# Kernel tuning notes

Measured on AMD Instinct MI355X. Metric: run time of the kernel, lower is better.

Reference implementation:

```python
import jax, jax.numpy as jnp
import numpy as np

D = 256          # input_dim (node embedding dim)
ATT_TIMES = 2
ATT_NUM = 2
DIN = D * ATT_NUM  # NTN input dim = 512
F = 16           # feature_map_dim


def setup_inputs() -> dict:
    key = jax.random.key(0)
    ks = jax.random.split(key, 10)
    x1 = jax.random.normal(ks[0], (120000, D), dtype=jnp.float32)
    x2 = jax.random.normal(ks[1], (100000, D), dtype=jnp.float32)
    # attention weight (glorot)
    W0 = jax.random.normal(ks[2], (D, D), dtype=jnp.float32) * (2.0 / (D + D)) ** 0.5
    # NTN params
    V = jax.random.normal(ks[3], (F, 2 * DIN), dtype=jnp.float32) * (2.0 / (F + 2 * DIN)) ** 0.5
    W = jax.random.normal(ks[4], (F, DIN, DIN), dtype=jnp.float32) * (2.0 / (DIN + DIN)) ** 0.5
    b = jax.random.normal(ks[5], (F,), dtype=jnp.float32)
    # projection MLP 16->8->4->2->1, torch Linear weights are (out, in)
    P0 = jax.random.normal(ks[6], (8, 16), dtype=jnp.float32) * (2.0 / (8 + 16)) ** 0.5
    P1 = jax.random.normal(ks[7], (4, 8), dtype=jnp.float32) * (2.0 / (4 + 8)) ** 0.5
    P2 = jax.random.normal(ks[8], (2, 4), dtype=jnp.float32) * (2.0 / (2 + 4)) ** 0.5
    P3 = jax.random.normal(ks[9], (1, 2), dtype=jnp.float32) * (2.0 / (1 + 2)) ** 0.5
    return {"x1": x1, "x2": x2, "W0": W0, "V": V, "W": W, "b": b,
            "P0": P0, "P1": P1, "P2": P2, "P3": P3}


def _attention(x, W0):
    # x: (N, D) -> (1, D*ATT_NUM) graph embedding.
    outs = []
    for _ in range(ATT_NUM):  # 'dot' style: same params each head (eye W), kept for faithfulness
        cur = x
        out = None
        for _ in range(ATT_TIMES):
            temp = jnp.mean(cur, axis=0, keepdims=True)          # (1, D)
            h_avg = jnp.tanh(temp @ W0)                          # att_weight=True
            att = jax.nn.sigmoid(cur @ h_avg.T)                  # (N, 1), W=eye in 'dot' style
            out = att.T @ cur                                    # (1, D)
            cur = cur * att
        outs.append(out)
    return jnp.concatenate(outs, axis=1)                         # (1, DIN)


def _ntn(g1, g2, V, W, b):
    # g1, g2: (1, DIN). Fused bilinear over all F feature maps.
    concat = jnp.concatenate([g1, g2], axis=1)                   # (1, 2*DIN)
    v_term = concat @ V.T                                        # (1, F)
    w_term = jnp.einsum('nd,fde,me->nf', g1, W, g2)              # (1, F)
    return jax.nn.sigmoid(v_term + w_term + b)                   # inneract = sigmoid


def reference(x1, x2, W0, V, W, b, P0, P1, P2, P3):
    g1 = _attention(x1, W0)
    g2 = _attention(x2, W0)
    x = _ntn(g1, g2, V, W, b)                                    # (1, F), branch 'an'
    for P in (P0, P1, P2, P3):                                   # Linear(no bias) + Sigmoid
        x = jax.nn.sigmoid(x @ P.T)
    return x                                                     # (1, 1)
```

## Files before the change

kernel.cpp:

```cpp
#include <hip/hip_runtime.h>
#include <math.h>

#define DD 256
#define REPS 8

#define OFF_SUMREP 0
#define OFF_H1P    4096
#define OFF_S1REP  4608
#define OFF_H2P    8704
#define OFF_OREP   9216
#define OFF_WTREP  13824
#define WS_FLOATS  13952
#define MIRROR_OFF_BYTES 65536

typedef float    f32x4 __attribute__((ext_vector_type(4)));
typedef float    f32x8 __attribute__((ext_vector_type(8)));
typedef _Float16 f16x4 __attribute__((ext_vector_type(4)));
typedef _Float16 f16x8 __attribute__((ext_vector_type(8)));

__device__ __forceinline__ float sigmoidf_(float x) { return 1.0f / (1.0f + __expf(-x)); }

__device__ __forceinline__ f32x8 ld8(const f16x8* p, size_t i) {
    return __builtin_convertvector(p[i], f32x8);
}
__device__ __forceinline__ f32x8 ld8(const f32x8* p, size_t i) { return p[i]; }

__device__ __forceinline__ float dot8(f32x8 a, f32x8 b) {
    f32x8 m = a * b;
    return ((m[0] + m[4]) + (m[1] + m[5])) + ((m[2] + m[6]) + (m[3] + m[7]));
}

__global__ void k_zero(float* __restrict__ ws) {
    int i = blockIdx.x * 256 + threadIdx.x;
    if (i < WS_FLOATS) ws[i] = 0.0f;
}

__device__ __forceinline__ void block_reduce_atomic4(f32x4 acc, int t, float* dst_base) {
    __shared__ f32x4 lds[256];
    lds[t] = acc;
    __syncthreads();
    if (t < 64) {
        f32x4 s = lds[t] + lds[t + 64] + lds[t + 128] + lds[t + 192];
        float* dst = dst_base + t * 4;
        atomicAdd(dst + 0, s.x); atomicAdd(dst + 1, s.y);
        atomicAdd(dst + 2, s.z); atomicAdd(dst + 3, s.w);
    }
}

__device__ __forceinline__ void block_reduce_atomic8(f32x8 acc, int t, float* dst_base) {
    __shared__ f32x8 lds8[256];
    lds8[t] = acc;
    __syncthreads();
    const float* lf = (const float*)lds8;
    float s = 0.f;
#pragma unroll
    for (int slot = 0; slot < 8; slot++) s += lf[slot * 256 + t];
    atomicAdd(dst_base + t, s);
}

template<bool WM>
__global__ void k_mean_t(const f32x4* __restrict__ x1, const f32x4* __restrict__ x2,
                         f16x4* __restrict__ m1, f16x4* __restrict__ m2,
                         int N1, int N2, float* __restrict__ ws) {
    int b = blockIdx.x, t = threadIdx.x;
    int inp = (b < 1024) ? 0 : 1;
    int bl = inp ? (b - 1024) : b;
    const f32x4* x = inp ? x2 : x1;
    f16x4* mm = inp ? m2 : m1;
    int N = inp ? N2 : N1;
    int col4 = t & 63, rg = t >> 6;
    int wid = bl * 4 + rg;
    const int S = 4096;
    f32x4 acc = {0.f, 0.f, 0.f, 0.f};
    int r = wid;
    for (; r + 3 * S < N; r += 4 * S) {
        size_t i0 = (size_t)r * 64 + col4;
        f32x4 v0 = x[i0];
        f32x4 v1 = x[i0 + (size_t)S * 64];
        f32x4 v2 = x[i0 + (size_t)2 * S * 64];
        f32x4 v3 = x[i0 + (size_t)3 * S * 64];
        if (WM) {
            mm[i0]                   = __builtin_convertvector(v0, f16x4);
            mm[i0 + (size_t)S * 64]  = __builtin_convertvector(v1, f16x4);
            mm[i0 + (size_t)2*S*64]  = __builtin_convertvector(v2, f16x4);
            mm[i0 + (size_t)3*S*64]  = __builtin_convertvector(v3, f16x4);
        }
        acc += (v0 + v1) + (v2 + v3);
    }
    for (; r < N; r += S) {
        size_t i0 = (size_t)r * 64 + col4;
        f32x4 v = x[i0];
        if (WM) mm[i0] = __builtin_convertvector(v, f16x4);
        acc += v;
    }
    block_reduce_atomic4(acc, t, ws + OFF_SUMREP + inp * (REPS * 256) + (bl & (REPS - 1)) * 256);
}

__global__ void k_hpart(const float* __restrict__ W0, float* __restrict__ ws,
                        int srcOff, int dstOff, int N1, int N2) {
    int inp = blockIdx.x >> 4, g = blockIdx.x & 15;
    int t = threadIdx.x;
    __shared__ float temp[16];
    if (t < 16) {
        const float* src = ws + srcOff + inp * (REPS * 256) + g * 16 + t;
        float s = 0.f;
#pragma unroll
        for (int r = 0; r < REPS; r++) s += src[r * 256];
        temp[t] = s * (1.0f / (float)(inp ? N2 : N1));
    }
    __syncthreads();
    float p = 0.f;
#pragma unroll
    for (int j = 0; j < 16; j++) p += temp[j] * W0[(g * 16 + j) * 256 + t];
    atomicAdd(ws + dstOff + inp * 256 + t, p);
}

template<typename T>
__global__ void k_att1_t(const T* __restrict__ b1, const T* __restrict__ b2,
                         int N1, int N2, float* __restrict__ ws) {
    int b = blockIdx.x, t = threadIdx.x;
    int inp = (b < 1024) ? 0 : 1;
    int bl = inp ? (b - 1024) : b;
    const T* x = inp ? b2 : b1;
    int N = inp ? N2 : N1;
    int lane = t & 63, w = t >> 6;
    int half = lane >> 5, l32 = lane & 31;
    f32x8 h1;
#pragma unroll
    for (int j = 0; j < 8; j++) h1[j] = tanhf(ws[OFF_H1P + inp * 256 + l32 * 8 + j]);
    f32x8 acc = {0.f, 0.f, 0.f, 0.f, 0.f, 0.f, 0.f, 0.f};
    int wid = bl * 4 + w;
    const int PS = 8192;
    int base = wid * 2;
    for (; base + PS + 1 < N; base += 2 * PS) {
        f32x8 va = ld8(x, (size_t)(base + half) * 32 + l32);
        f32x8 vb = ld8(x, (size_t)(base + PS + half) * 32 + l32);
        float da = dot8(va, h1), db = dot8(vb, h1);
#pragma unroll
        for (int off = 16; off; off >>= 1) {
            da += __shfl_xor(da, off, 64);
            db += __shfl_xor(db, off, 64);
        }
        acc += sigmoidf_(da) * va + sigmoidf_(db) * vb;
    }
    for (; base + 1 < N; base += PS) {
        f32x8 v = ld8(x, (size_t)(base + half) * 32 + l32);
        float d = dot8(v, h1);
#pragma unroll
        for (int off = 16; off; off >>= 1) d += __shfl_xor(d, off, 64);
        acc += sigmoidf_(d) * v;
    }
    if (base < N && half == 0) {
        f32x8 v = ld8(x, (size_t)base * 32 + l32);
        float d = dot8(v, h1);
#pragma unroll
        for (int off = 16; off; off >>= 1) d += __shfl_xor(d, off, 64);
        acc += sigmoidf_(d) * v;
    }
    block_reduce_atomic8(acc, t, ws + OFF_S1REP + inp * (REPS * 256) + (bl & (REPS - 1)) * 256);
}

template<typename T>
__global__ void k_att2_t(const T* __restrict__ b1, const T* __restrict__ b2,
                         int N1, int N2, float* __restrict__ ws) {
    int b = blockIdx.x, t = threadIdx.x;
    int inp = (b < 1024) ? 0 : 1;
    int bl = inp ? (b - 1024) : b;
    const T* x = inp ? b2 : b1;
    int N = inp ? N2 : N1;
    int lane = t & 63, w = t >> 6;
    int half = lane >> 5, l32 = lane & 31;
    f32x8 h1, h2;
#pragma unroll
    for (int j = 0; j < 8; j++) {
        h1[j] = tanhf(ws[OFF_H1P + inp * 256 + l32 * 8 + j]);
        h2[j] = tanhf(ws[OFF_H2P + inp * 256 + l32 * 8 + j]);
    }
    f32x8 acc = {0.f, 0.f, 0.f, 0.f, 0.f, 0.f, 0.f, 0.f};
    int wid = bl * 4 + w;
    const int PS = 8192;
    int base = wid * 2;
    for (; base + PS + 1 < N; base += 2 * PS) {
        f32x8 va = ld8(x, (size_t)(base + half) * 32 + l32);
        f32x8 vb = ld8(x, (size_t)(base + PS + half) * 32 + l32);
        float da = dot8(va, h1), ea = dot8(va, h2);
        float db = dot8(vb, h1), eb = dot8(vb, h2);
#pragma unroll
        for (int off = 16; off; off >>= 1) {
            da += __shfl_xor(da, off, 64); ea += __shfl_xor(ea, off, 64);
            db += __shfl_xor(db, off, 64); eb += __shfl_xor(eb, off, 64);
        }
        float a1a = sigmoidf_(da);
        float a1b = sigmoidf_(db);
        acc += (a1a * sigmoidf_(a1a * ea)) * va + (a1b * sigmoidf_(a1b * eb)) * vb;
    }
    for (; base + 1 < N; base += PS) {
        f32x8 v = ld8(x, (size_t)(base + half) * 32 + l32);
        float d = dot8(v, h1), e = dot8(v, h2);
#pragma unroll
        for (int off = 16; off; off >>= 1) {
            d += __shfl_xor(d, off, 64); e += __shfl_xor(e, off, 64);
        }
        float a1 = sigmoidf_(d);
        acc += (a1 * sigmoidf_(a1 * e)) * v;
    }
    if (base < N && half == 0) {
        f32x8 v = ld8(x, (size_t)base * 32 + l32);
        float d = dot8(v, h1), e = dot8(v, h2);
#pragma unroll
        for (int off = 16; off; off >>= 1) {
            d += __shfl_xor(d, off, 64); e += __shfl_xor(e, off, 64);
        }
        float a1 = sigmoidf_(d);
        acc += (a1 * sigmoidf_(a1 * e)) * v;
    }
    block_reduce_atomic8(acc, t, ws + OFF_OREP + inp * (REPS * 256) + (bl & (REPS - 1)) * 256);
}

__global__ void __launch_bounds__(256, 4)
k_ntn(const float* __restrict__ W, float* __restrict__ ws) {
    __shared__ __align__(16) float o_l[512];
    int b = blockIdx.x, t = threadIdx.x;
    {
        float s0 = 0.f, s1 = 0.f;
#pragma unroll
        for (int r2 = 0; r2 < REPS; r2++) {
            s0 += ws[OFF_OREP + r2 * 256 + t];
            s1 += ws[OFF_OREP + REPS * 256 + r2 * 256 + t];
        }
        o_l[t] = s0; o_l[256 + t] = s1;
    }
    __syncthreads();
    int lane = t & 63, w = t >> 6;
    f32x4 o2f = ((const f32x4*)(o_l + 256))[lane];
    int g = b * 4 + w;
    const f32x4* W4 = (const f32x4*)W;
    float wt[4];
    int fidx[4];
#pragma unroll
    for (int u = 0; u < 4; u++) {
        int row = g + u * 2048;
        const f32x4* q = W4 + (size_t)row * 128 + lane;
        f32x4 m = (q[0] + q[64]) * o2f;
        float p = (m.x + m.y) + (m.z + m.w);
#pragma unroll
        for (int off = 32; off; off >>= 1) p += __shfl_xor(p, off, 64);
        wt[u] = o_l[row & 255] * p;
        fidx[u] = row >> 9;
    }
    if (lane == 0) {
        float* dst = ws + OFF_WTREP + (b & (REPS - 1)) * 16;
#pragma unroll
        for (int u = 0; u < 4; u++) atomicAdd(dst + fidx[u], wt[u]);
    }
}

__global__ void k_final(const float* __restrict__ V, const float* __restrict__ bb,
                        const float* __restrict__ P0, const float* __restrict__ P1,
                        const float* __restrict__ P2, const float* __restrict__ P3,
                        float* __restrict__ ws, float* __restrict__ out) {
    int t = threadIdx.x;
    __shared__ float o_l[512];
    {
        float s0 = 0.f, s1 = 0.f;
#pragma unroll
        for (int r2 = 0; r2 < REPS; r2++) {
            s0 += ws[OFF_OREP + r2 * 256 + t];
            s1 += ws[OFF_OREP + REPS * 256 + r2 * 256 + t];
        }
        o_l[t] = s0; o_l[256 + t] = s1;
    }
    __syncthreads();
    int f = t >> 4, j = t & 15;
    float p = 0.f;
    for (int k = j; k < 1024; k += 16) {
        float cv = (k < 512) ? o_l[k & 255] : o_l[256 + (k & 255)];
        p += cv * V[f * 1024 + k];
    }
    __shared__ float red[256];
    __shared__ float sv[16];
    red[t] = p;
    __syncthreads();
    if (t < 16) {
        float v = 0.f;
#pragma unroll
        for (int q = 0; q < 16; q++) v += red[t * 16 + q];
        float wt = 0.f;
#pragma unroll
        for (int r = 0; r < REPS; r++) wt += ws[OFF_WTREP + r * 16 + t];
        sv[t] = sigmoidf_(v + wt + bb[t]);
    }
    __syncthreads();
    if (t == 0) {
        float y0[8], y1[4], y2[2];
#pragma unroll
        for (int i = 0; i < 8; i++) {
            float s = 0.f;
            for (int k = 0; k < 16; k++) s += P0[i * 16 + k] * sv[k];
            y0[i] = sigmoidf_(s);
        }
#pragma unroll
        for (int i = 0; i < 4; i++) {
            float s = 0.f;
            for (int k = 0; k < 8; k++) s += P1[i * 8 + k] * y0[k];
            y1[i] = sigmoidf_(s);
        }
#pragma unroll
        for (int i = 0; i < 2; i++) {
            float s = 0.f;
            for (int k = 0; k < 4; k++) s += P2[i * 4 + k] * y1[k];
            y2[i] = sigmoidf_(s);
        }
        out[0] = sigmoidf_(P3[0] * y2[0] + P3[1] * y2[1]);
    }
}

extern "C" void kernel_launch(void* const* d_in, const int* in_sizes, int n_in,
                              void* d_out, int out_size, void* d_ws, size_t ws_size,
                              hipStream_t stream) {
    const float* x1 = (const float*)d_in[0];
    const float* x2 = (const float*)d_in[1];
    const float* W0 = (const float*)d_in[2];
    const float* V  = (const float*)d_in[3];
    const float* W  = (const float*)d_in[4];
    const float* b  = (const float*)d_in[5];
    const float* P0 = (const float*)d_in[6];
    const float* P1 = (const float*)d_in[7];
    const float* P2 = (const float*)d_in[8];
    const float* P3 = (const float*)d_in[9];
    float* ws  = (float*)d_ws;
    float* out = (float*)d_out;
    int N1 = in_sizes[0] / DD;
    int N2 = in_sizes[1] / DD;

    const f32x4* x1v = (const f32x4*)x1;
    const f32x4* x2v = (const f32x4*)x2;
    f16x4* m1 = (f16x4*)((char*)d_ws + MIRROR_OFF_BYTES);
    f16x4* m2 = m1 + (size_t)N1 * 64;
    size_t need = (size_t)MIRROR_OFF_BYTES + ((size_t)N1 + N2) * DD * sizeof(_Float16);
    bool use_mirror = ws_size >= need;

    k_zero <<<55, 256, 0, stream>>>(ws);
    if (use_mirror) {
        k_mean_t<true>  <<<2048, 256, 0, stream>>>(x1v, x2v, m1, m2, N1, N2, ws);
        k_hpart         <<<32,   256, 0, stream>>>(W0, ws, OFF_SUMREP, OFF_H1P, N1, N2);
        k_att1_t<f16x8> <<<2048, 256, 0, stream>>>((const f16x8*)m1, (const f16x8*)m2, N1, N2, ws);
        k_hpart         <<<32,   256, 0, stream>>>(W0, ws, OFF_S1REP, OFF_H2P, N1, N2);
        k_att2_t<f16x8> <<<2048, 256, 0, stream>>>((const f16x8*)m1, (const f16x8*)m2, N1, N2, ws);
    } else {
        k_mean_t<false> <<<2048, 256, 0, stream>>>(x1v, x2v, nullptr, nullptr, N1, N2, ws);
        k_hpart         <<<32,   256, 0, stream>>>(W0, ws, OFF_SUMREP, OFF_H1P, N1, N2);
        k_att1_t<f32x8> <<<2048, 256, 0, stream>>>((const f32x8*)x1, (const f32x8*)x2, N1, N2, ws);
        k_hpart         <<<32,   256, 0, stream>>>(W0, ws, OFF_S1REP, OFF_H2P, N1, N2);
        k_att2_t<f32x8> <<<2048, 256, 0, stream>>>((const f32x8*)x1, (const f32x8*)x2, N1, N2, ws);
    }
    k_ntn  <<<512, 256, 0, stream>>>(W, ws);
    k_final<<<1,   256, 0, stream>>>(V, b, P0, P1, P2, P3, ws, out);
}
```

Measured before the change: 415.0 us.

## Give each block a contiguous row chunk in mean and attention passes

Replaces grid-strided row assignment, where consecutive blocks interleave rows across the whole matrix, with a contiguous chunk of about N/1024 rows per block in the mean, att1 and att2 kernels. Each block streams one contiguous region, which is meant to improve DRAM page and cache locality. The att1 loop is also unrolled to four rows per wave per iteration to put more loads in flight. The cost is a little extra bounds arithmetic per block and possible imbalance when N is not a multiple of 1024.

Result: no change. 418.9 us (+1.0%).

```diff
diff --git a/kernel.cpp b/kernel.cpp
--- a/kernel.cpp
+++ b/kernel.cpp
@@ -68,26 +68,28 @@
     const f32x4* x = inp ? x2 : x1;
     f16x4* mm = inp ? m2 : m1;
     int N = inp ? N2 : N1;
+    int C = (N + 1023) >> 10;
+    int r0 = bl * C;
+    int r1 = r0 + C; if (r1 > N) r1 = N;
+    if (r0 > N) r0 = N;
     int col4 = t & 63, rg = t >> 6;
-    int wid = bl * 4 + rg;
-    const int S = 4096;
     f32x4 acc = {0.f, 0.f, 0.f, 0.f};
-    int r = wid;
-    for (; r + 3 * S < N; r += 4 * S) {
+    int r = r0 + rg;
+    for (; r + 12 < r1; r += 16) {
         size_t i0 = (size_t)r * 64 + col4;
         f32x4 v0 = x[i0];
-        f32x4 v1 = x[i0 + (size_t)S * 64];
-        f32x4 v2 = x[i0 + (size_t)2 * S * 64];
-        f32x4 v3 = x[i0 + (size_t)3 * S * 64];
+        f32x4 v1 = x[i0 + 256];
+        f32x4 v2 = x[i0 + 512];
+        f32x4 v3 = x[i0 + 768];
         if (WM) {
-            mm[i0]                   = __builtin_convertvector(v0, f16x4);
-            mm[i0 + (size_t)S * 64]  = __builtin_convertvector(v1, f16x4);
-            mm[i0 + (size_t)2*S*64]  = __builtin_convertvector(v2, f16x4);
-            mm[i0 + (size_t)3*S*64]  = __builtin_convertvector(v3, f16x4);
+            mm[i0]       = __builtin_convertvector(v0, f16x4);
+            mm[i0 + 256] = __builtin_convertvector(v1, f16x4);
+            mm[i0 + 512] = __builtin_convertvector(v2, f16x4);
+            mm[i0 + 768] = __builtin_convertvector(v3, f16x4);
         }
         acc += (v0 + v1) + (v2 + v3);
     }
-    for (; r < N; r += S) {
+    for (; r < r1; r += 4) {
         size_t i0 = (size_t)r * 64 + col4;
         f32x4 v = x[i0];
         if (WM) mm[i0] = __builtin_convertvector(v, f16x4);
@@ -123,35 +125,37 @@
     int bl = inp ? (b - 1024) : b;
     const T* x = inp ? b2 : b1;
     int N = inp ? N2 : N1;
+    int C = (N + 1023) >> 10;
+    int r0 = bl * C;
+    int r1 = r0 + C; if (r1 > N) r1 = N;
+    if (r0 > N) r0 = N;
     int lane = t & 63, w = t >> 6;
     int half = lane >> 5, l32 = lane & 31;
     f32x8 h1;
 #pragma unroll
     for (int j = 0; j < 8; j++) h1[j] = tanhf(ws[OFF_H1P + inp * 256 + l32 * 8 + j]);
     f32x8 acc = {0.f, 0.f, 0.f, 0.f, 0.f, 0.f, 0.f, 0.f};
-    int wid = bl * 4 + w;
-    const int PS = 8192;
-    int base = wid * 2;
-    for (; base + PS + 1 < N; base += 2 * PS) {
-        f32x8 va = ld8(x, (size_t)(base + half) * 32 + l32);
-        f32x8 vb = ld8(x, (size_t)(base + PS + half) * 32 + l32);
+    int rr = r0;
+    for (; rr + 32 <= r1; rr += 32) {
+        int ra = rr + 2 * w + half;
+        f32x8 va = ld8(x, (size_t)ra * 32 + l32);
+        f32x8 vb = ld8(x, (size_t)(ra + 8) * 32 + l32);
+        f32x8 vc = ld8(x, (size_t)(ra + 16) * 32 + l32);
+        f32x8 vd = ld8(x, (size_t)(ra + 24) * 32 + l32);
         float da = dot8(va, h1), db = dot8(vb, h1);
+        float dc = dot8(vc, h1), dd = dot8(vd, h1);
 #pragma unroll
         for (int off = 16; off; off >>= 1) {
             da += __shfl_xor(da, off, 64);
             db += __shfl_xor(db, off, 64);
+            dc += __shfl_xor(dc, off, 64);
+            dd += __shfl_xor(dd, off, 64);
         }
         acc += sigmoidf_(da) * va + sigmoidf_(db) * vb;
-    }
-    for (; base + 1 < N; base += PS) {
-        f32x8 v = ld8(x, (size_t)(base + half) * 32 + l32);
-        float d = dot8(v, h1);
-#pragma unroll
-        for (int off = 16; off; off >>= 1) d += __shfl_xor(d, off, 64);
-        acc += sigmoidf_(d) * v;
-    }
-    if (base < N && half == 0) {
-        f32x8 v = ld8(x, (size_t)base * 32 + l32);
+        acc += sigmoidf_(dc) * vc + sigmoidf_(dd) * vd;
+    }
+    for (int ra = rr + 2 * w + half; ra < r1; ra += 8) {
+        f32x8 v = ld8(x, (size_t)ra * 32 + l32);
         float d = dot8(v, h1);
 #pragma unroll
         for (int off = 16; off; off >>= 1) d += __shfl_xor(d, off, 64);
@@ -168,6 +172,10 @@
     int bl = inp ? (b - 1024) : b;
     const T* x = inp ? b2 : b1;
     int N = inp ? N2 : N1;
+    int C = (N + 1023) >> 10;
+    int r0 = bl * C;
+    int r1 = r0 + C; if (r1 > N) r1 = N;
+    if (r0 > N) r0 = N;
     int lane = t & 63, w = t >> 6;
     int half = lane >> 5, l32 = lane & 31;
     f32x8 h1, h2;
@@ -177,12 +185,11 @@
         h2[j] = tanhf(ws[OFF_H2P + inp * 256 + l32 * 8 + j]);
     }
     f32x8 acc = {0.f, 0.f, 0.f, 0.f, 0.f, 0.f, 0.f, 0.f};
-    int wid = bl * 4 + w;
-    const int PS = 8192;
-    int base = wid * 2;
-    for (; base + PS + 1 < N; base += 2 * PS) {
-        f32x8 va = ld8(x, (size_t)(base + half) * 32 + l32);
-        f32x8 vb = ld8(x, (size_t)(base + PS + half) * 32 + l32);
+    int rr = r0;
+    for (; rr + 16 <= r1; rr += 16) {
+        int ra = rr + 2 * w + half;
+        f32x8 va = ld8(x, (size_t)ra * 32 + l32);
+        f32x8 vb = ld8(x, (size_t)(ra + 8) * 32 + l32);
         float da = dot8(va, h1), ea = dot8(va, h2);
         float db = dot8(vb, h1), eb = dot8(vb, h2);
 #pragma unroll
@@ -194,18 +201,8 @@
         float a1b = sigmoidf_(db);
         acc += (a1a * sigmoidf_(a1a * ea)) * va + (a1b * sigmoidf_(a1b * eb)) * vb;
     }
-    for (; base + 1 < N; base += PS) {
-        f32x8 v = ld8(x, (size_t)(base + half) * 32 + l32);
-        float d = dot8(v, h1), e = dot8(v, h2);
-#pragma unroll
-        for (int off = 16; off; off >>= 1) {
-            d += __shfl_xor(d, off, 64); e += __shfl_xor(e, off, 64);
-        }
-        float a1 = sigmoidf_(d);
-        acc += (a1 * sigmoidf_(a1 * e)) * v;
-    }
-    if (base < N && half == 0) {
-        f32x8 v = ld8(x, (size_t)base * 32 + l32);
+    for (int ra = rr + 2 * w + half; ra < r1; ra += 8) {
+        f32x8 v = ld8(x, (size_t)ra * 32 + l32);
         float d = dot8(v, h1), e = dot8(v, h2);
 #pragma unroll
         for (int off = 16; off; off >>= 1) {
```
